# Optimization experiments

Hardware: AMD Instinct MI355X
Metric: run time of the kernel (lower is better)

Reference implementation:

```python
import jax, jax.numpy as jnp
import numpy as np
from math import sqrt

DK = 64  # head dim from __init__ default


def setup_inputs() -> dict:
    key = jax.random.key(0)
    k1, k2, k3 = jax.random.split(key, 3)
    N, DV = 8192, 64
    Q = jax.random.normal(k1, (N, DK), dtype=jnp.float32)
    K = jax.random.normal(k2, (N, DK), dtype=jnp.float32)
    V = jax.random.normal(k3, (N, DV), dtype=jnp.float32)
    return {"Q": Q, "K": K, "V": V}


def reference(Q, K, V):
    # scores: [Nq, Nk]
    scores = jnp.einsum('qd,kd->qk', Q, K) * (1.0 / sqrt(DK))
    # softmax over key axis (torch nn.Softmax(dim=1) on 2D scores)
    attn = jax.nn.softmax(scores, axis=1)
    return jnp.einsum('qk,kv->qv', attn, V)
```

## Files before the change

### kernel.cpp

```cpp
#include <hip/hip_runtime.h>
#include <math.h>


typedef __bf16 bf16;
typedef __attribute__((ext_vector_type(8)))  __bf16 bf16x8;
typedef __attribute__((ext_vector_type(16))) float  f32x16;

#define DKc 64
#define DVc 64
#define TK  64
#define QB  128
#define SCALE_LOG2E 0.1803368801111204f
#define M2FIX 8.0f

__device__ __forceinline__ f32x16 mfma_bf16(bf16x8 a, bf16x8 b, f32x16 c) {
    return __builtin_amdgcn_mfma_f32_32x32x16_bf16(a, b, c, 0, 0, 0);
}
__device__ __forceinline__ int rp4(int r) {
    return ((r >> 2) & 1) * 8 + (r & 3) + ((r >> 3) << 2);
}

__global__ __launch_bounds__(256)
void prepass(const float* __restrict__ K, const float* __restrict__ V,
             bf16* __restrict__ Kf, bf16* __restrict__ Vf, int N) {
    const int b = blockIdx.x, tid = threadIdx.x;
    const int ntile = N / TK;
    if (b < ntile) {
        const size_t tbase = (size_t)b * 4096;
#pragma unroll
        for (int w = 0; w < 2; ++w) {
            int idx = w * 256 + tid;
            int sub = idx >> 8, f = (idx >> 6) & 3, l = idx & 63;
            int h = l >> 5, c = l & 31;
            const float* src = K + (size_t)(b * 64 + sub * 32 + c) * DKc + f * 16 + h * 8;
            float4 a  = *(const float4*)src;
            float4 b4 = *(const float4*)(src + 4);
            bf16x8 o;
            o[0]=(bf16)a.x;  o[1]=(bf16)a.y;  o[2]=(bf16)a.z;  o[3]=(bf16)a.w;
            o[4]=(bf16)b4.x; o[5]=(bf16)b4.y; o[6]=(bf16)b4.z; o[7]=(bf16)b4.w;
            *(bf16x8*)(Kf + tbase + (size_t)idx * 8) = o;
        }
    } else {
        const int T = b - ntile;
        __shared__ float sT[64][65];
#pragma unroll
        for (int p = 0; p < 4; ++p) {
            int fi = p * 256 + tid;
            int e0 = fi * 4;
            int key = e0 >> 6, dv = e0 & 63;
            float4 v = ((const float4*)(V + (size_t)T * 64 * DVc))[fi];
            sT[dv + 0][key] = v.x; sT[dv + 1][key] = v.y;
            sT[dv + 2][key] = v.z; sT[dv + 3][key] = v.w;
        }
        __syncthreads();
        const size_t tbase = (size_t)T * 4096;
#pragma unroll
        for (int w = 0; w < 2; ++w) {
            int idx = w * 256 + tid;
            int sub = idx >> 8, kb = (idx >> 6) & 3, l = idx & 63;
            int h = l >> 5, c = l & 31;
            bf16x8 o;
#pragma unroll
            for (int j = 0; j < 8; ++j)
                o[j] = (bf16)sT[sub * 32 + c][kb * 16 + rp4(h * 8 + j)];
            *(bf16x8*)(Vf + tbase + (size_t)idx * 8) = o;
        }
    }
}

#define STEP(kf)                                                              \
    {                                                                         \
        f32x16 d0 = {0}, d1 = {0};                                            \
        __builtin_amdgcn_s_setprio(1);                                        \
        _Pragma("unroll")                                                     \
        for (int f = 0; f < 4; ++f) {                                         \
            d0 = mfma_bf16(kf[2*f],   qf[f], d0);                             \
            d1 = mfma_bf16(kf[2*f+1], qf[f], d1);                             \
        }                                                                     \
        __builtin_amdgcn_s_setprio(0);                                        \
        float ps0 = 0.f, ps1 = 0.f, ps2 = 0.f, ps3 = 0.f;                     \
        _Pragma("unroll")                                                     \
        for (int r = 0; r < 16; r += 4) {                                     \
            d0[r]   = __builtin_amdgcn_exp2f(d0[r]   - M2FIX); ps0 += d0[r];  \
            d0[r+1] = __builtin_amdgcn_exp2f(d0[r+1] - M2FIX); ps1 += d0[r+1];\
            d0[r+2] = __builtin_amdgcn_exp2f(d0[r+2] - M2FIX); ps2 += d0[r+2];\
            d0[r+3] = __builtin_amdgcn_exp2f(d0[r+3] - M2FIX); ps3 += d0[r+3];\
            d1[r]   = __builtin_amdgcn_exp2f(d1[r]   - M2FIX); ps0 += d1[r];  \
            d1[r+1] = __builtin_amdgcn_exp2f(d1[r+1] - M2FIX); ps1 += d1[r+1];\
            d1[r+2] = __builtin_amdgcn_exp2f(d1[r+2] - M2FIX); ps2 += d1[r+2];\
            d1[r+3] = __builtin_amdgcn_exp2f(d1[r+3] - M2FIX); ps3 += d1[r+3];\
        }                                                                     \
        float psum = (ps0 + ps1) + (ps2 + ps3);                               \
        psum += __shfl_xor(psum, 32);                                         \
        lsum += psum;                                                         \
        bf16x8 pa[4];                                                         \
        _Pragma("unroll")                                                     \
        for (int j = 0; j < 8; ++j) {                                         \
            pa[0][j] = (bf16)d0[j];                                           \
            pa[1][j] = (bf16)d0[8 + j];                                       \
            pa[2][j] = (bf16)d1[j];                                           \
            pa[3][j] = (bf16)d1[8 + j];                                       \
        }                                                                     \
        __builtin_amdgcn_s_setprio(1);                                        \
        _Pragma("unroll")                                                     \
        for (int kb = 0; kb < 4; ++kb) {                                      \
            O0 = mfma_bf16(pa[kb], vf[2*kb],   O0);                           \
            O1 = mfma_bf16(pa[kb], vf[2*kb+1], O1);                           \
        }                                                                     \
        __builtin_amdgcn_s_setprio(0);                                        \
    }

__global__ __launch_bounds__(256, 2)
void attn_fwd_mfma(const float* __restrict__ Q, const bf16* __restrict__ Kf,
                   const bf16* __restrict__ Vf,
                   float* __restrict__ Opart, float* __restrict__ Lpart,
                   float* __restrict__ Out, int N, int splits, int chunk) {
    const int tid  = threadIdx.x;
    const int wid  = tid >> 6;
    const int lane = tid & 63;
    const int l31  = lane & 31;
    const int h    = lane >> 5;

    const int qbase = blockIdx.x * QB + wid * 32;
    const int q     = qbase + l31;
    const int sp    = blockIdx.y;

    bf16x8 qf[4];
#pragma unroll
    for (int f = 0; f < 4; ++f) {
        const float* qp = Q + (size_t)q * DKc + f * 16 + h * 8;
        float4 a = *(const float4*)qp;
        float4 b = *(const float4*)(qp + 4);
        qf[f][0] = (bf16)(a.x * SCALE_LOG2E); qf[f][1] = (bf16)(a.y * SCALE_LOG2E);
        qf[f][2] = (bf16)(a.z * SCALE_LOG2E); qf[f][3] = (bf16)(a.w * SCALE_LOG2E);
        qf[f][4] = (bf16)(b.x * SCALE_LOG2E); qf[f][5] = (bf16)(b.y * SCALE_LOG2E);
        qf[f][6] = (bf16)(b.z * SCALE_LOG2E); qf[f][7] = (bf16)(b.w * SCALE_LOG2E);
    }

    f32x16 O0 = {0}, O1 = {0};
    float lsum = 0.f;

    const int k0 = sp * chunk;
    int k1 = k0 + chunk; if (k1 > N) k1 = N;
    const int tile0  = k0 >> 6;
    const int ntiles = (k1 - k0) >> 6;

    auto loadK = [&](bf16x8* kf, int tile) {
        const bf16* Kt = Kf + (size_t)tile * 4096;
#pragma unroll
        for (int f = 0; f < 4; ++f) {
            kf[2*f]   = *(const bf16x8*)(Kt + (size_t)(f * 64 + lane) * 8);
            kf[2*f+1] = *(const bf16x8*)(Kt + (size_t)(256 + f * 64 + lane) * 8);
        }
    };
    auto loadV = [&](bf16x8* vf, int tile) {
        const bf16* Vt = Vf + (size_t)tile * 4096;
#pragma unroll
        for (int kb = 0; kb < 4; ++kb) {
            vf[2*kb]   = *(const bf16x8*)(Vt + (size_t)(kb * 64 + lane) * 8);
            vf[2*kb+1] = *(const bf16x8*)(Vt + (size_t)(256 + kb * 64 + lane) * 8);
        }
    };

    bf16x8 kA[8], kB[8], vf[8];
    loadK(kA, tile0);

    for (int it = 0; it < ntiles; it += 2) {
        loadV(vf, tile0 + it);
        if (it + 1 < ntiles) loadK(kB, tile0 + it + 1);
        STEP(kA)
        if (it + 1 < ntiles) {
            loadV(vf, tile0 + it + 1);
            if (it + 2 < ntiles) loadK(kA, tile0 + it + 2);
            STEP(kB)
        }
    }

    if (splits == 1) {
        float inv = 1.f / lsum;
#pragma unroll
        for (int r = 0; r < 16; ++r) {
            int qr = (r & 3) + 8 * (r >> 2) + 4 * h;
            float fr = __shfl(inv, (lane & 32) | qr);
            int qq = qbase + qr;
            Out[(size_t)qq * DVc + l31]      = O0[r] * fr;
            Out[(size_t)qq * DVc + 32 + l31] = O1[r] * fr;
        }
    } else {
#pragma unroll
        for (int r = 0; r < 16; ++r) {
            int qr = (r & 3) + 8 * (r >> 2) + 4 * h;
            int qq = qbase + qr;
            size_t off = ((size_t)sp * N + qq) * DVc;
            Opart[off + l31]      = O0[r];
            Opart[off + 32 + l31] = O1[r];
        }
        if (lane < 32) Lpart[(size_t)sp * N + q] = lsum;
    }
}

__global__ __launch_bounds__(256)
void attn_combine(const float* __restrict__ Opart, const float* __restrict__ Lpart,
                  float* __restrict__ Out, int N, int splits) {
    const int t  = blockIdx.x * blockDim.x + threadIdx.x;
    const int q  = t >> 4;
    const int d4 = t & 15;

    float4 acc = make_float4(0.f, 0.f, 0.f, 0.f);
    float  L = 0.f;
    for (int s = 0; s < splits; ++s) {
        L += Lpart[(size_t)s * N + q];
        float4 ov = *(const float4*)(Opart + ((size_t)s * N + q) * DVc + d4 * 4);
        acc.x += ov.x; acc.y += ov.y; acc.z += ov.z; acc.w += ov.w;
    }
    float inv = 1.f / L;
    *(float4*)(Out + (size_t)q * DVc + d4 * 4) =
        make_float4(acc.x * inv, acc.y * inv, acc.z * inv, acc.w * inv);
}

extern "C" void kernel_launch(void* const* d_in, const int* in_sizes, int n_in,
                              void* d_out, int out_size, void* d_ws, size_t ws_size,
                              hipStream_t stream) {
    const float* Q = (const float*)d_in[0];
    const float* K = (const float*)d_in[1];
    const float* V = (const float*)d_in[2];
    float* Out = (float*)d_out;

    const int N = in_sizes[0] / DKc;

    const size_t bfbytes = (size_t)N * DKc * sizeof(short);
    bf16* Kf = (bf16*)d_ws;
    bf16* Vf = (bf16*)((char*)d_ws + bfbytes);
    char* rest = (char*)d_ws + 2 * bfbytes;
    size_t rest_sz = (ws_size > 2 * bfbytes) ? ws_size - 2 * bfbytes : 0;

    int splits = 16;
    while (splits > 1 &&
           (size_t)splits * (size_t)N * (DVc + 1) * sizeof(float) > rest_sz)
        splits >>= 1;
    int chunk = (N + splits - 1) / splits;
    chunk = ((chunk + TK - 1) / TK) * TK;

    float* Opart = (float*)rest;
    float* Lpart = Opart + (size_t)splits * N * DVc;

    const int ntile = N / TK;
    prepass<<<2 * ntile, 256, 0, stream>>>(K, V, Kf, Vf, N);

    dim3 grid(N / QB, splits);
    attn_fwd_mfma<<<grid, 256, 0, stream>>>(Q, Kf, Vf, Opart, Lpart, Out,
                                            N, splits, chunk);
    if (splits > 1) {
        int total = N * 16;
        attn_combine<<<total / 256, 256, 0, stream>>>(Opart, Lpart, Out, N, splits);
    }
}
```

Before: 93.75 us.

## Interleave exp and PV MFMAs per half-tile, defer row-sum reduction, halve splits

Each step now splits the softmax exponentiation into two halves, issuing the PV MFMAs for the first half before exponentiating the second half so the exp work can overlap matrix-core work. The per-tile partial sums and cross-lane shuffle are moved out of the loop into four running accumulators reduced once at the end. The split-K count drops from 16 to 8, which halves partial-output traffic and combine work but gives fewer blocks to fill the GPU.

```diff
diff --git a/kernel.cpp b/kernel.cpp
--- a/kernel.cpp
+++ b/kernel.cpp
@@ -78,35 +78,43 @@
             d1 = mfma_bf16(kf[2*f+1], qf[f], d1);                             \
         }                                                                     \
         __builtin_amdgcn_s_setprio(0);                                        \
-        float ps0 = 0.f, ps1 = 0.f, ps2 = 0.f, ps3 = 0.f;                     \
+                                                      \
         _Pragma("unroll")                                                     \
         for (int r = 0; r < 16; r += 4) {                                     \
             d0[r]   = __builtin_amdgcn_exp2f(d0[r]   - M2FIX); ps0 += d0[r];  \
             d0[r+1] = __builtin_amdgcn_exp2f(d0[r+1] - M2FIX); ps1 += d0[r+1];\
             d0[r+2] = __builtin_amdgcn_exp2f(d0[r+2] - M2FIX); ps2 += d0[r+2];\
             d0[r+3] = __builtin_amdgcn_exp2f(d0[r+3] - M2FIX); ps3 += d0[r+3];\
+        }                                                                     \
+        bf16x8 pa0, pa1;                                                      \
+        _Pragma("unroll")                                                     \
+        for (int j = 0; j < 8; ++j) { pa0[j] = (bf16)d0[j];                   \
+                                      pa1[j] = (bf16)d0[8 + j]; }             \
+          \
+        __builtin_amdgcn_s_setprio(1);                                        \
+        O0 = mfma_bf16(pa0, vf[0], O0);                                       \
+        O1 = mfma_bf16(pa0, vf[1], O1);                                       \
+        O0 = mfma_bf16(pa1, vf[2], O0);                                       \
+        O1 = mfma_bf16(pa1, vf[3], O1);                                       \
+        __builtin_amdgcn_s_setprio(0);                                        \
+                                                     \
+        _Pragma("unroll")                                                     \
+        for (int r = 0; r < 16; r += 4) {                                     \
             d1[r]   = __builtin_amdgcn_exp2f(d1[r]   - M2FIX); ps0 += d1[r];  \
             d1[r+1] = __builtin_amdgcn_exp2f(d1[r+1] - M2FIX); ps1 += d1[r+1];\
             d1[r+2] = __builtin_amdgcn_exp2f(d1[r+2] - M2FIX); ps2 += d1[r+2];\
             d1[r+3] = __builtin_amdgcn_exp2f(d1[r+3] - M2FIX); ps3 += d1[r+3];\
         }                                                                     \
-        float psum = (ps0 + ps1) + (ps2 + ps3);                               \
-        psum += __shfl_xor(psum, 32);                                         \
-        lsum += psum;                                                         \
-        bf16x8 pa[4];                                                         \
-        _Pragma("unroll")                                                     \
-        for (int j = 0; j < 8; ++j) {                                         \
-            pa[0][j] = (bf16)d0[j];                                           \
-            pa[1][j] = (bf16)d0[8 + j];                                       \
-            pa[2][j] = (bf16)d1[j];                                           \
-            pa[3][j] = (bf16)d1[8 + j];                                       \
-        }                                                                     \
+        bf16x8 pa2, pa3;                                                      \
+        _Pragma("unroll")                                                     \
+        for (int j = 0; j < 8; ++j) { pa2[j] = (bf16)d1[j];                   \
+                                      pa3[j] = (bf16)d1[8 + j]; }             \
+                                                 \
         __builtin_amdgcn_s_setprio(1);                                        \
-        _Pragma("unroll")                                                     \
-        for (int kb = 0; kb < 4; ++kb) {                                      \
-            O0 = mfma_bf16(pa[kb], vf[2*kb],   O0);                           \
-            O1 = mfma_bf16(pa[kb], vf[2*kb+1], O1);                           \
-        }                                                                     \
+        O0 = mfma_bf16(pa2, vf[4], O0);                                       \
+        O1 = mfma_bf16(pa2, vf[5], O1);                                       \
+        O0 = mfma_bf16(pa3, vf[6], O0);                                       \
+        O1 = mfma_bf16(pa3, vf[7], O1);                                       \
         __builtin_amdgcn_s_setprio(0);                                        \
     }
 
@@ -138,7 +146,7 @@
     }
 
     f32x16 O0 = {0}, O1 = {0};
-    float lsum = 0.f;
+    float ps0 = 0.f, ps1 = 0.f, ps2 = 0.f, ps3 = 0.f;
 
     const int k0 = sp * chunk;
     int k1 = k0 + chunk; if (k1 > N) k1 = N;
@@ -176,6 +184,9 @@
         }
     }
 
+    float lsum = (ps0 + ps1) + (ps2 + ps3);
+    lsum += __shfl_xor(lsum, 32);
+
     if (splits == 1) {
         float inv = 1.f / lsum;
 #pragma unroll
@@ -234,7 +245,7 @@
     char* rest = (char*)d_ws + 2 * bfbytes;
     size_t rest_sz = (ws_size > 2 * bfbytes) ? ws_size - 2 * bfbytes : 0;
 
-    int splits = 16;
+    int splits = 8;
     while (splits > 1 &&
            (size_t)splits * (size_t)N * (DVc + 1) * sizeof(float) > rest_sz)
         splits >>= 1;
```

Result: faster. 89.55 us (-4.5%).
